# Optimization experiments

Measured on AMD Instinct MI355X. Metric: run time of the kernel, lower is better.

Reference implementation:

```python
import jax, jax.numpy as jnp
import numpy as np

N, F, H, R, B, L, C, E, NB = 8192, 512, 256, 16, 32, 256, 7, 262144, 30
D = F + H


def setup_inputs() -> dict:
    ks = jax.random.split(jax.random.key(0), 16)
    g = lambda k, shape, fan: jax.random.normal(k, shape, jnp.float32) / np.sqrt(fan)
    return {
        "x": jax.random.normal(ks[0], (N, F), jnp.float32),
        "edge_index": jax.random.randint(ks[1], (2, E), 0, N),
        "edge_norm": jax.random.uniform(ks[2], (E,), jnp.float32),
        "edge_type": jax.random.randint(ks[3], (E,), 0, R),
        "seq_lengths": jnp.full((B,), L, dtype=jnp.int32),
        "umask": jnp.ones((B, L), jnp.float32),
        "nodal_attn": 1,
        "avec": 0,
        "basis": g(ks[4], (NB, F, H), F),
        "comp": g(ks[5], (R, NB), NB),
        "root1": g(ks[6], (F, H), F),
        "bias1": jnp.zeros((H,), jnp.float32),
        "w_rel": g(ks[7], (H, H), H),
        "b_rel": jnp.zeros((H,), jnp.float32),
        "w_root": g(ks[8], (H, H), H),
        "w_att": g(ks[9], (D, D), D),
        "b_att": jnp.zeros((D,), jnp.float32),
        "w_lin": g(ks[10], (D, H), D),
        "b_lin": jnp.zeros((H,), jnp.float32),
        "w_fc": g(ks[11], (H, C), H),
        "b_fc": jnp.zeros((C,), jnp.float32),
    }


def reference(x, edge_index, edge_norm, edge_type, seq_lengths, umask,
              nodal_attn, avec, basis, comp, root1, bias1, w_rel, b_rel,
              w_root, w_att, b_att, w_lin, b_lin, w_fc, b_fc):
    n = x.shape[0]
    r = comp.shape[0]
    src, dst = edge_index[0], edge_index[1]
    # ---- RGCNConv (num_bases basis decomposition, mean aggregation per relation, root + bias)
    W = jnp.einsum('rb,bfh->rfh', comp, basis)             # [R,F,H]
    xw = jnp.einsum('nf,rfh->nrh', x, W)                   # [N,R,H]
    msg = xw[src, edge_type]                               # [E,H] gather per edge
    seg = dst * r + edge_type                              # per (node, relation) segment
    cnt = jax.ops.segment_sum(jnp.ones((msg.shape[0],), msg.dtype), seg, num_segments=n * r)
    msg = msg / jnp.maximum(cnt[seg], 1.0)[:, None]
    out1 = jax.ops.segment_sum(msg, dst, num_segments=n) + x @ root1 + bias1
    # ---- GraphConv (add aggregation): W_rel * sum_j h_j + b_rel + W_root * h_i
    agg2 = jax.ops.segment_sum(out1[src], dst, num_segments=n)
    out2 = agg2 @ w_rel + b_rel + out1 @ w_root
    emotions = jnp.concatenate([x, out2], axis=-1)          # [N, F+H]
    if int(nodal_attn):
        seq = np.asarray(seq_lengths)                       # static conversation lengths
        starts = np.concatenate([[0], np.cumsum(seq)[:-1]])
        lmax = int(seq.max())
        rows = [jnp.pad(jax.lax.dynamic_slice_in_dim(emotions, int(s), int(l)),
                        ((0, lmax - int(l)), (0, 0)))
                for s, l in zip(starts, seq)]
        M = jnp.stack(rows, 0).transpose(1, 0, 2)           # [L, B, D]
        mask = umask                                        # [B, L]
        # MatchingAttention 'general2', vectorized over all timesteps t
        X = M @ w_att + b_att                               # transform(x_t) for every t: [L,B,D]
        Mm = M * mask.T[:, :, None]                         # mask memory over seq dim
        scores = jnp.einsum('tbd,sbd->tbs', X, Mm) * mask[None]
        a = jax.nn.softmax(jnp.tanh(scores), axis=-1) * mask[None]
        a = a / jnp.sum(a, axis=-1, keepdims=True)
        att = jnp.einsum('tbs,sbd->tbd', a, M)              # [L,B,D]
        hidden = jax.nn.relu(att @ w_lin + b_lin)
    else:
        hidden = jax.nn.relu(emotions @ w_lin + b_lin)
    # dropout is identity in eval mode
    logits = hidden @ w_fc + b_fc
    if int(avec):
        return logits
    return jax.nn.log_softmax(logits, axis=1)  # faithful: torch uses dim=1
```

## Files before the change

kernel.cpp:

```cpp
#include <hip/hip_runtime.h>
#include <hip/hip_bf16.h>

#define NN 8192
#define FF 512
#define HH 256
#define RR 16
#define BB 32
#define LL 256
#define CC 7
#define EE 262144
#define NBASE 30
#define DD 768

constexpr int FLAG_BIAS = 1, FLAG_RELU = 4, FLAG_TANH = 8,
              FLAG_SPLITOUT = 16, FLAG_TAILOUT = 32, FLAG_TAIL2 = 64;

typedef __attribute__((ext_vector_type(8))) short bf16x8;
typedef __attribute__((ext_vector_type(4))) float f32x4;

__global__ __launch_bounds__(256) void detect_dtype(const unsigned short* __restrict__ xs,
                                                    int* __restrict__ flag) {
  __shared__ int red[256];
  int cnt = 0;
  for (int i = threadIdx.x * 2; i < 8192; i += 512) {
    unsigned short u = xs[i];
    int e = (u >> 7) & 0xFF;
    if (e >= 0xC0) cnt++;
  }
  red[threadIdx.x] = cnt;
  __syncthreads();
  for (int s = 128; s > 0; s >>= 1) {
    if (threadIdx.x < s) red[threadIdx.x] += red[threadIdx.x + s];
    __syncthreads();
  }
  if (threadIdx.x == 0) flag[0] = (red[0] > 16) ? 1 : 0;
}

struct PSeg {
  const void* src;
  float* dst;
  __hip_bfloat16* hi;
  __hip_bfloat16* lo;
  __hip_bfloat16* hi2;
  __hip_bfloat16* lo2;
  long n;
  int R, C, ld, off;
  int type;
  int zero;
};
struct PTable {
  PSeg seg[16];
  int count;
  long total;
};

__global__ __launch_bounds__(256) void prep_all(PTable t, const int* __restrict__ flag) {
  const int fp32 = flag[0];
  for (long i = (long)blockIdx.x * 256 + threadIdx.x; i < t.total;
       i += (long)gridDim.x * 256) {
    long off = i;
    int s = 0;
    while (off >= t.seg[s].n) { off -= t.seg[s].n; s++; }
    const PSeg& sg = t.seg[s];
    if (sg.type == 0) {
      float v = 0.f;
      if (!sg.zero)
        v = fp32 ? ((const float*)sg.src)[off]
                 : __bfloat162float(((const __hip_bfloat16*)sg.src)[off]);
      if (sg.dst) sg.dst[off] = v;
      if (sg.hi) {
        __hip_bfloat16 h = __float2bfloat16(v);
        __hip_bfloat16 l = __float2bfloat16(v - __bfloat162float(h));
        sg.hi[off] = h;
        sg.lo[off] = l;
        if (sg.hi2) {
          long d2 = (off >> 9) * DD + (off & 511);
          sg.hi2[d2] = h;
          sg.lo2[d2] = l;
        }
      }
    } else {
      int r = (int)(off % sg.R), c = (int)(off / sg.R);
      float v = fp32 ? ((const float*)sg.src)[(long)r * sg.C + c]
                     : __bfloat162float(((const __hip_bfloat16*)sg.src)[(long)r * sg.C + c]);
      __hip_bfloat16 h = __float2bfloat16(v);
      long d = (long)c * sg.ld + sg.off + r;
      sg.hi[d] = h;
      sg.lo[d] = __float2bfloat16(v - __bfloat162float(h));
    }
  }
}

__global__ __launch_bounds__(256) void wt_gemm(
    const float* __restrict__ basis, const float* __restrict__ comp,
    float* __restrict__ wt_nat) {
  __shared__ float cs[RR * NBASE];
  int tid = threadIdx.x;
  for (int i = tid; i < RR * NBASE; i += 256) cs[i] = comp[i];
  __syncthreads();
  long col = (long)blockIdx.x * 256 + tid;
  float acc[RR] = {};
  for (int b = 0; b < NBASE; ++b) {
    float v = basis[(long)b * 131072 + col];
#pragma unroll
    for (int r = 0; r < RR; ++r) acc[r] += cs[r * NBASE + b] * v;
  }
#pragma unroll
  for (int r = 0; r < RR; ++r) wt_nat[(long)r * 131072 + col] = acc[r];
}

__global__ __launch_bounds__(256) void wt_transpose(
    const float* __restrict__ wt_nat,
    __hip_bfloat16* __restrict__ hi, __hip_bfloat16* __restrict__ lo) {
  __shared__ float t[32][33];
  const int r = blockIdx.z;
  const int f0 = blockIdx.y * 32, h0 = blockIdx.x * 32;
  const int c = threadIdx.x & 31, rw = threadIdx.x >> 5;
  const float* src = wt_nat + ((long)r * 512 + f0) * 256 + h0;
#pragma unroll
  for (int i = 0; i < 4; ++i)
    t[rw + i * 8][c] = src[(long)(rw + i * 8) * 256 + c];
  __syncthreads();
#pragma unroll
  for (int i = 0; i < 4; ++i) {
    int hh = rw + i * 8;
    float v = t[c][hh];
    long orow = (long)(r * 256 + h0 + hh) * 512 + f0 + c;
    __hip_bfloat16 hv = __float2bfloat16(v);
    hi[orow] = hv;
    lo[orow] = __float2bfloat16(v - __bfloat162float(hv));
  }
}

__device__ __forceinline__ void gload_lds16(const void* g, void* l) {
  __builtin_amdgcn_global_load_lds(
      (const __attribute__((address_space(1))) unsigned int*)g,
      (__attribute__((address_space(3))) unsigned int*)l, 16, 0, 0);
}

__global__ __launch_bounds__(256, 3) void mfma_dual(
    const __hip_bfloat16* __restrict__ A, const __hip_bfloat16* __restrict__ Alo,
    const __hip_bfloat16* __restrict__ Bt, const __hip_bfloat16* __restrict__ Btlo,
    const float* __restrict__ bias, float* __restrict__ C, float* __restrict__ Ct,
    __hip_bfloat16* __restrict__ Chi, __hip_bfloat16* __restrict__ Clo,
    __hip_bfloat16* __restrict__ Chi2, __hip_bfloat16* __restrict__ Clo2,
    int K, int ldc, long sA, long sB, long sC, int flags) {
  __shared__ __hip_bfloat16 Ah[128 * 32];
  __shared__ __hip_bfloat16 Bh[128 * 32];
  __shared__ __hip_bfloat16 Al[128 * 32];
  __shared__ __hip_bfloat16 Bl[128 * 32];
  const int tid = threadIdx.x;
  const int w = tid >> 6, lane = tid & 63;
  const long z = blockIdx.z;
  const long row0 = (long)blockIdx.y * 128, col0 = (long)blockIdx.x * 128;
  const int wm = w & 1, wn = w >> 1;
  const int srow0 = (w * 128 + lane) >> 2;
  const int srow1 = (w * 128 + 64 + lane) >> 2;
  const int kch = (lane & 3) * 8;
  const int fr = lane & 15, q = lane >> 4;
  const bool hasAlo = (Alo != nullptr);
  const __hip_bfloat16* Az = A + z * sA;
  const __hip_bfloat16* Alz = hasAlo ? (Alo + z * sA) : nullptr;
  const __hip_bfloat16* Bz = Bt + z * sB;
  const __hip_bfloat16* Blz = Btlo + z * sB;
  const long aoff0 = (row0 + srow0) * K + kch, aoff1 = (row0 + srow1) * K + kch;
  const long boff0 = (col0 + srow0) * K + kch, boff1 = (col0 + srow1) * K + kch;
  f32x4 acc[4][4] = {};
  for (int k0 = 0; k0 < K; k0 += 32) {
    gload_lds16(Az + aoff0 + k0, Ah + w * 1024);
    gload_lds16(Az + aoff1 + k0, Ah + w * 1024 + 512);
    gload_lds16(Bz + boff0 + k0, Bh + w * 1024);
    gload_lds16(Bz + boff1 + k0, Bh + w * 1024 + 512);
    gload_lds16(Blz + boff0 + k0, Bl + w * 1024);
    gload_lds16(Blz + boff1 + k0, Bl + w * 1024 + 512);
    if (hasAlo) {
      gload_lds16(Alz + aoff0 + k0, Al + w * 1024);
      gload_lds16(Alz + aoff1 + k0, Al + w * 1024 + 512);
    }
    __syncthreads();
    bf16x8 ah[4], bh[4], bl[4];
#pragma unroll
    for (int i = 0; i < 4; ++i) {
      ah[i] = *(const bf16x8*)&Ah[(wm * 64 + i * 16 + fr) * 32 + q * 8];
      bh[i] = *(const bf16x8*)&Bh[(wn * 64 + i * 16 + fr) * 32 + q * 8];
      bl[i] = *(const bf16x8*)&Bl[(wn * 64 + i * 16 + fr) * 32 + q * 8];
    }
#pragma unroll
    for (int i = 0; i < 4; ++i)
#pragma unroll
      for (int j = 0; j < 4; ++j) {
        acc[i][j] = __builtin_amdgcn_mfma_f32_16x16x32_bf16(ah[i], bh[j], acc[i][j], 0, 0, 0);
        acc[i][j] = __builtin_amdgcn_mfma_f32_16x16x32_bf16(ah[i], bl[j], acc[i][j], 0, 0, 0);
      }
    if (hasAlo) {
      bf16x8 al[4];
#pragma unroll
      for (int i = 0; i < 4; ++i)
        al[i] = *(const bf16x8*)&Al[(wm * 64 + i * 16 + fr) * 32 + q * 8];
#pragma unroll
      for (int i = 0; i < 4; ++i)
#pragma unroll
        for (int j = 0; j < 4; ++j)
          acc[i][j] = __builtin_amdgcn_mfma_f32_16x16x32_bf16(al[i], bh[j], acc[i][j], 0, 0, 0);
    }
    __syncthreads();
  }
  const int cr = (lane >> 4) * 4, cc = lane & 15;
  float* Cz = C ? (C + z * sC) : nullptr;
  __hip_bfloat16* Chz = Chi ? (Chi + z * sC) : nullptr;
  __hip_bfloat16* Clz = Clo ? (Clo + z * sC) : nullptr;
#pragma unroll
  for (int i = 0; i < 4; ++i) {
    long rbase = row0 + wm * 64 + i * 16 + cr;
#pragma unroll
    for (int j = 0; j < 4; ++j) {
      long col = col0 + wn * 64 + j * 16 + cc;
      float bv = (flags & FLAG_BIAS) ? bias[col] : 0.f;
#pragma unroll
      for (int r = 0; r < 4; ++r) {
        float v = acc[i][j][r] + bv;
        if (flags & FLAG_RELU) v = fmaxf(v, 0.f);
        if (flags & FLAG_TANH) v = tanhf(v);
        long row = rbase + r;
        if ((flags & FLAG_TAIL2) && col >= 768) {
          long off2 = (row >> 8) * 65536 + (col - 768) * 256 + (row & 255);
          __hip_bfloat16 hv = __float2bfloat16(v);
          Chi2[off2] = hv;
          Clo2[off2] = __float2bfloat16(v - __bfloat162float(hv));
        } else if (flags & FLAG_SPLITOUT) {
          long off = row * ldc + col;
          __hip_bfloat16 hv = __float2bfloat16(v);
          Chz[off] = hv;
          Clz[off] = __float2bfloat16(v - __bfloat162float(hv));
        } else if ((flags & FLAG_TAILOUT) && col >= 4096) {
          Ct[row * 256 + (col - 4096)] = v;
        } else {
          Cz[row * ldc + col] = v;
        }
      }
    }
  }
}

__global__ __launch_bounds__(256) void count_edges(
    const int* __restrict__ ei, const int* __restrict__ et, float* __restrict__ cnt) {
  int e = blockIdx.x * 256 + threadIdx.x;
  if (e < EE) atomicAdd(&cnt[ei[EE + e] * RR + et[e]], 1.0f);
}

__global__ __launch_bounds__(256) void scan_rowptr(
    const float* __restrict__ cntf, int* __restrict__ rowptr, int* __restrict__ fill) {
  __shared__ int part[256];
  int tid = threadIdx.x;
  int base = tid * 32;
  int local[32];
  int s = 0;
  for (int i = 0; i < 32; ++i) {
    local[i] = s;
    const float* c = &cntf[(base + i) * RR];
    int d = 0;
#pragma unroll
    for (int r = 0; r < RR; ++r) d += (int)c[r];
    s += d;
  }
  part[tid] = s;
  __syncthreads();
  for (int off = 1; off < 256; off <<= 1) {
    int v = (tid >= off) ? part[tid - off] : 0;
    __syncthreads();
    part[tid] += v;
    __syncthreads();
  }
  int prev = (tid == 0) ? 0 : part[tid - 1];
  for (int i = 0; i < 32; ++i) rowptr[base + i] = prev + local[i];
  if (tid == 255) rowptr[8192] = part[255];
  for (int i = tid; i < 8192; i += 256) fill[i] = 0;
}

__global__ __launch_bounds__(256) void edge_fill(
    const int* __restrict__ ei, const int* __restrict__ et,
    const int* __restrict__ rowptr, int* __restrict__ fill, int* __restrict__ eidx) {
  int e = blockIdx.x * 256 + threadIdx.x;
  if (e < EE) {
    int dst = ei[EE + e];
    int pos = rowptr[dst] + atomicAdd(&fill[dst], 1);
    eidx[pos] = ei[e] | (et[e] << 16);
  }
}

__global__ __launch_bounds__(256) void rgcn_gather(
    const int* __restrict__ rowptr, const int* __restrict__ eidx,
    const float* __restrict__ cntf, const float* __restrict__ xw,
    float* __restrict__ out1, __hip_bfloat16* __restrict__ a2o1_hi,
    __hip_bfloat16* __restrict__ a2o1_lo) {
  const int dst = blockIdx.x;
  const int h = threadIdx.x;
  __shared__ float inv[RR];
  __shared__ int se[256];
  if (h < RR) inv[h] = 1.0f / fmaxf(cntf[dst * RR + h], 1.0f);
  const int beg = rowptr[dst], end = rowptr[dst + 1];
  float a0 = 0.f, a1 = 0.f, a2 = 0.f, a3 = 0.f;
  for (int c0 = beg; c0 < end; c0 += 256) {
    int n = min(256, end - c0);
    __syncthreads();
    if (h < n) se[h] = eidx[c0 + h];
    __syncthreads();
    int i = 0;
    for (; i + 4 <= n; i += 4) {
      int p0 = se[i], p1 = se[i + 1], p2 = se[i + 2], p3 = se[i + 3];
      float v0 = xw[((long)(p0 & 0xFFFF) << 12) + ((p0 >> 16) << 8) + h];
      float v1 = xw[((long)(p1 & 0xFFFF) << 12) + ((p1 >> 16) << 8) + h];
      float v2 = xw[((long)(p2 & 0xFFFF) << 12) + ((p2 >> 16) << 8) + h];
      float v3 = xw[((long)(p3 & 0xFFFF) << 12) + ((p3 >> 16) << 8) + h];
      a0 += v0 * inv[p0 >> 16];
      a1 += v1 * inv[p1 >> 16];
      a2 += v2 * inv[p2 >> 16];
      a3 += v3 * inv[p3 >> 16];
    }
    for (; i < n; ++i) {
      int pk = se[i];
      a0 += xw[((long)(pk & 0xFFFF) << 12) + ((pk >> 16) << 8) + h] * inv[pk >> 16];
    }
  }
  float tot = out1[((long)dst << 8) + h] + ((a0 + a1) + (a2 + a3));
  out1[((long)dst << 8) + h] = tot;
  __hip_bfloat16 hv = __float2bfloat16(tot);
  long d = (long)dst * 512 + 256 + h;
  a2o1_hi[d] = hv;
  a2o1_lo[d] = __float2bfloat16(tot - __bfloat162float(hv));
}

__global__ __launch_bounds__(256) void graphconv_gather(
    const int* __restrict__ rowptr, const int* __restrict__ eidx,
    const float* __restrict__ out1, __hip_bfloat16* __restrict__ a2o1_hi,
    __hip_bfloat16* __restrict__ a2o1_lo) {
  const int dst = blockIdx.x;
  const int h = threadIdx.x;
  __shared__ int se[256];
  const int beg = rowptr[dst], end = rowptr[dst + 1];
  float a0 = 0.f, a1 = 0.f, a2 = 0.f, a3 = 0.f;
  for (int c0 = beg; c0 < end; c0 += 256) {
    int n = min(256, end - c0);
    __syncthreads();
    if (h < n) se[h] = eidx[c0 + h];
    __syncthreads();
    int i = 0;
    for (; i + 4 <= n; i += 4) {
      a0 += out1[((long)(se[i] & 0xFFFF) << 8) + h];
      a1 += out1[((long)(se[i + 1] & 0xFFFF) << 8) + h];
      a2 += out1[((long)(se[i + 2] & 0xFFFF) << 8) + h];
      a3 += out1[((long)(se[i + 3] & 0xFFFF) << 8) + h];
    }
    for (; i < n; ++i) a0 += out1[((long)(se[i] & 0xFFFF) << 8) + h];
  }
  float acc = (a0 + a1) + (a2 + a3);
  __hip_bfloat16 hv = __float2bfloat16(acc);
  long d = (long)dst * 512 + h;
  a2o1_hi[d] = hv;
  a2o1_lo[d] = __float2bfloat16(acc - __bfloat162float(hv));
}

__global__ __launch_bounds__(256) void softmax256(const float* __restrict__ S,
                                                  __hip_bfloat16* __restrict__ Ab) {
  __shared__ float red[256];
  long row = blockIdx.x;
  const float* p = S + row * 256;
  int t = threadIdx.x;
  float v = p[t];
  red[t] = v;
  __syncthreads();
  for (int s = 128; s > 0; s >>= 1) {
    if (t < s) red[t] = fmaxf(red[t], red[t + s]);
    __syncthreads();
  }
  float m = red[0];
  __syncthreads();
  float e = __expf(v - m);
  red[t] = e;
  __syncthreads();
  for (int s = 128; s > 0; s >>= 1) {
    if (t < s) red[t] += red[t + s];
    __syncthreads();
  }
  Ab[row * 256 + t] = __float2bfloat16(e / red[0]);
}

__global__ __launch_bounds__(256) void logits_lsm(
    const float* __restrict__ hidden, const float* __restrict__ w_fc,
    const float* __restrict__ b_fc, void* __restrict__ out_v,
    const int* __restrict__ flag) {
  __shared__ float wf[256 * 7];
  __shared__ float lg[224];
  __shared__ float corr[7];
  int t = blockIdx.x;
  int tid = threadIdx.x;
  for (int i = tid; i < 256 * 7; i += 256) wf[i] = w_fc[i];
  __syncthreads();
  if (tid < 224) {
    int b = tid / 7, c = tid % 7;
    const float* hr = hidden + ((long)((b << 8) + t) << 8);
    float s = b_fc[c];
    for (int k = 0; k < 256; ++k) s += hr[k] * wf[k * 7 + c];
    lg[tid] = s;
  }
  __syncthreads();
  if (tid < 7) {
    float m = -1e30f;
    for (int b = 0; b < BB; ++b) m = fmaxf(m, lg[b * 7 + tid]);
    float sum = 0.f;
    for (int b = 0; b < BB; ++b) sum += __expf(lg[b * 7 + tid] - m);
    corr[tid] = m + logf(sum);
  }
  __syncthreads();
  if (tid < 224) {
    float v = lg[tid] - corr[tid % 7];
    if (flag[0]) ((float*)out_v)[t * 224 + tid] = v;
    else ((__hip_bfloat16*)out_v)[t * 224 + tid] = __float2bfloat16(v);
  }
}

extern "C" void kernel_launch(void* const* d_in, const int* in_sizes, int n_in,
                              void* d_out, int out_size, void* d_ws, size_t ws_size,
                              hipStream_t stream) {
  const int* ei = (const int*)d_in[1];
  const int* et = (const int*)d_in[3];

  float* ws = (float*)d_ws;
  int* flag = (int*)d_ws;
  float* p = ws + 16;
  auto alloc = [&](long nf) { float* r = p; p += nf; return r; };
  float* w_fc_f = alloc(1792);
  float* b_rel_f = alloc(256);
  float* biasx = alloc(4352);
  float* battx = alloc(1024);
  float* b_lin_f = alloc(256);
  float* b_fc_f = alloc(16);
  __hip_bfloat16* x_hi = (__hip_bfloat16*)alloc(2097152);
  __hip_bfloat16* x_lo = (__hip_bfloat16*)alloc(2097152);
  __hip_bfloat16* wae_hi = (__hip_bfloat16*)alloc(393216);
  __hip_bfloat16* wae_lo = (__hip_bfloat16*)alloc(393216);
  __hip_bfloat16* wrr_hi = (__hip_bfloat16*)alloc(65536);
  __hip_bfloat16* wrr_lo = (__hip_bfloat16*)alloc(65536);
  __hip_bfloat16* wtc_hi = (__hip_bfloat16*)alloc(1114112);
  __hip_bfloat16* wtc_lo = (__hip_bfloat16*)alloc(1114112);
  float* basis_f = alloc(3932160);
  float* comp_f = alloc(512);
  float* xw = alloc(33554432);
  float* cnt = alloc(131072);
  float* out1 = alloc(2097152);
  __hip_bfloat16* a2o1_hi = (__hip_bfloat16*)alloc(2097152);
  __hip_bfloat16* a2o1_lo = (__hip_bfloat16*)alloc(2097152);
  float* hidden = alloc(2097152);
  int* rowptr = (int*)alloc(8208);
  int* fillc = (int*)alloc(8192);
  int* eidx = (int*)alloc(262144);
  float* wt_nat = xw;
  float* em = xw;
  __hip_bfloat16* emwT_hi = (__hip_bfloat16*)(em + 2097152);
  __hip_bfloat16* emwT_lo = (__hip_bfloat16*)(em + 3145728);
  __hip_bfloat16* em_hi = (__hip_bfloat16*)(em + 6291456);
  __hip_bfloat16* em_lo = (__hip_bfloat16*)(em + 9437184);
  __hip_bfloat16* X_hi = (__hip_bfloat16*)(em + 12582912);
  __hip_bfloat16* X_lo = (__hip_bfloat16*)(em + 15728640);
  float* scores = em + 18874368;
  __hip_bfloat16* a_b16 = (__hip_bfloat16*)(em + 20971520);

  detect_dtype<<<1, 256, 0, stream>>>((const unsigned short*)d_in[0], flag);
  PTable T{};
  long tot = 0;
  int ns = 0;
  auto segL = [&](const void* s, float* d, __hip_bfloat16* hi, __hip_bfloat16* lo,
                  __hip_bfloat16* hi2, __hip_bfloat16* lo2, long n, int z) {
    T.seg[ns] = PSeg{s, d, hi, lo, hi2, lo2, n, 0, 0, 0, 0, 0, z};
    ns++; tot += n;
  };
  auto segT = [&](const void* s, __hip_bfloat16* hi, __hip_bfloat16* lo,
                  int R, int C, int ld, int off) {
    T.seg[ns] = PSeg{s, nullptr, hi, lo, nullptr, nullptr, (long)R * C, R, C, ld, off, 1, 0};
    ns++; tot += (long)R * C;
  };
  segL(d_in[0], nullptr, x_hi, x_lo, nullptr, nullptr, NN * FF, 0);
  segL(d_in[8], basis_f, nullptr, nullptr, nullptr, nullptr, NBASE * FF * HH, 0);
  segL(d_in[9], comp_f, nullptr, nullptr, nullptr, nullptr, RR * NBASE, 0);
  segL(d_in[13], b_rel_f, nullptr, nullptr, nullptr, nullptr, HH, 0);
  segL(d_in[16], battx, nullptr, nullptr, nullptr, nullptr, DD, 0);
  segL(nullptr, battx + DD, nullptr, nullptr, nullptr, nullptr, 256, 1);
  segL(d_in[18], b_lin_f, nullptr, nullptr, nullptr, nullptr, HH, 0);
  segL(d_in[19], w_fc_f, nullptr, nullptr, nullptr, nullptr, HH * CC, 0);
  segL(d_in[20], b_fc_f, nullptr, nullptr, nullptr, nullptr, CC, 0);
  segL(nullptr, biasx, nullptr, nullptr, nullptr, nullptr, 4096, 1);
  segL(d_in[11], biasx + 4096, nullptr, nullptr, nullptr, nullptr, HH, 0);
  segT(d_in[15], wae_hi, wae_lo, DD, DD, DD, 0);
  segT(d_in[17], wae_hi + 768 * 768, wae_lo + 768 * 768, DD, HH, DD, 0);
  segT(d_in[10], wtc_hi + 4096 * 512, wtc_lo + 4096 * 512, FF, HH, FF, 0);
  segT(d_in[12], wrr_hi, wrr_lo, HH, HH, 512, 0);
  segT(d_in[14], wrr_hi, wrr_lo, HH, HH, 512, 256);
  T.count = ns;
  T.total = tot;
  prep_all<<<4096, 256, 0, stream>>>(T, flag);

  wt_gemm<<<131072 / 256, 256, 0, stream>>>(basis_f, comp_f, wt_nat);
  wt_transpose<<<dim3(8, 16, 16), 256, 0, stream>>>(wt_nat, wtc_hi, wtc_lo);
  mfma_dual<<<dim3(34, 64, 1), 256, 0, stream>>>(
      x_hi, x_lo, wtc_hi, wtc_lo, biasx, xw, out1, nullptr, nullptr, nullptr, nullptr,
      FF, 4096, 0, 0, 0, FLAG_BIAS | FLAG_TAILOUT);
  hipMemsetAsync(cnt, 0, 131072 * sizeof(float), stream);
  count_edges<<<EE / 256, 256, 0, stream>>>(ei, et, cnt);
  scan_rowptr<<<1, 256, 0, stream>>>(cnt, rowptr, fillc);
  edge_fill<<<EE / 256, 256, 0, stream>>>(ei, et, rowptr, fillc, eidx);
  rgcn_gather<<<NN, 256, 0, stream>>>(rowptr, eidx, cnt, xw, out1, a2o1_hi, a2o1_lo);
  graphconv_gather<<<NN, 256, 0, stream>>>(rowptr, eidx, out1, a2o1_hi, a2o1_lo);
  {
    PTable T2{};
    T2.seg[0] = PSeg{nullptr, nullptr, nullptr, nullptr, nullptr, nullptr,
                     (long)NN * FF, 0, 0, 0, 0, 2, 0};
  }
  {
    struct { const __hip_bfloat16 *xh, *xl; __hip_bfloat16 *eh, *el; } args{x_hi, x_lo, em_hi, em_lo};
  }
  extern __global__ void copy_xsplit_k(const __hip_bfloat16*, const __hip_bfloat16*,
                                       __hip_bfloat16*, __hip_bfloat16*);
  copy_xsplit_k<<<(NN * FF) / 256, 256, 0, stream>>>(x_hi, x_lo, em_hi, em_lo);
  mfma_dual<<<dim3(2, 64, 1), 256, 0, stream>>>(
      a2o1_hi, a2o1_lo, wrr_hi, wrr_lo, b_rel_f, nullptr, nullptr,
      em_hi + 512, em_lo + 512, nullptr, nullptr, 512, DD, 0, 0, 0,
      FLAG_BIAS | FLAG_SPLITOUT);
  mfma_dual<<<dim3(8, 64, 1), 256, 0, stream>>>(
      em_hi, em_lo, wae_hi, wae_lo, battx, nullptr, nullptr, X_hi, X_lo,
      emwT_hi, emwT_lo, DD, DD, 0, 0, 0, FLAG_BIAS | FLAG_SPLITOUT | FLAG_TAIL2);
  mfma_dual<<<dim3(2, 2, BB), 256, 0, stream>>>(
      X_hi, X_lo, em_hi, em_lo, nullptr, scores, nullptr, nullptr, nullptr,
      nullptr, nullptr, DD, LL, (long)LL * DD, (long)LL * DD, (long)LL * LL, FLAG_TANH);
  softmax256<<<BB * LL, 256, 0, stream>>>(scores, a_b16);
  mfma_dual<<<dim3(2, 2, BB), 256, 0, stream>>>(
      a_b16, nullptr, emwT_hi, emwT_lo, b_lin_f, hidden, nullptr, nullptr, nullptr,
      nullptr, nullptr, LL, HH, (long)LL * LL, (long)LL * HH, (long)LL * HH,
      FLAG_BIAS | FLAG_RELU);
  logits_lsm<<<LL, 256, 0, stream>>>(hidden, w_fc_f, b_fc_f, d_out, flag);
}

__global__ __launch_bounds__(256) void copy_xsplit_k(
    const __hip_bfloat16* __restrict__ xh, const __hip_bfloat16* __restrict__ xl,
    __hip_bfloat16* __restrict__ eh, __hip_bfloat16* __restrict__ el) {
  int idx = blockIdx.x * 256 + threadIdx.x;
  int n = idx >> 9, f = idx & 511;
  long d = (long)n * DD + f;
  eh[d] = xh[idx];
  el[d] = xl[idx];
}
```

Baseline: 616.3 us.

## Add 256x256-tile 8-wave split-bf16 MFMA GEMM with pipelined LDS loads for big GEMMs

Introduces mfma_dual8, a 512-thread kernel computing 256x256 output tiles with three bf16 MFMA passes (hi*hi, hi*lo, lo*hi), double-buffered direct global-to-LDS loads interleaved with compute phases, XOR-swizzled LDS reads, setprio around MFMA bursts and a grid swizzle for L2 locality. It replaces the older kernel for the two largest GEMMs (x times the relation weights and the attention transform), aiming to raise data reuse per tile and overlap memory with math. It also removes some dead scaffolding blocks. The larger tile gives fewer workgroups (544 and 128), which may leave some CUs idle and adds register pressure.

```diff
diff --git a/kernel.cpp b/kernel.cpp
--- a/kernel.cpp
+++ b/kernel.cpp
@@ -236,6 +236,143 @@
           Ct[row * 256 + (col - 4096)] = v;
         } else {
           Cz[row * ldc + col] = v;
+        }
+      }
+    }
+  }
+}
+
+__device__ __forceinline__ void rd4(bf16x8 (&d)[4], const __hip_bfloat16* t,
+                                    int rbase, int ro) {
+#pragma unroll
+  for (int i = 0; i < 4; ++i)
+    d[i] = *(const bf16x8*)&t[(rbase + i * 16) * 32 + ro];
+}
+
+__device__ __forceinline__ void mm16(f32x4 (&acc)[8][4], int g,
+                                     const bf16x8 (&a)[4], const bf16x8 (&b)[4]) {
+#pragma unroll
+  for (int i = 0; i < 4; ++i)
+#pragma unroll
+    for (int j = 0; j < 4; ++j)
+      acc[g * 4 + i][j] =
+          __builtin_amdgcn_mfma_f32_16x16x32_bf16(a[i], b[j], acc[g * 4 + i][j], 0, 0, 0);
+}
+
+#define P_TAIL(g_)                                   \
+  __builtin_amdgcn_s_barrier();                      \
+  asm volatile("s_waitcnt lgkmcnt(0)" ::: "memory"); \
+  __builtin_amdgcn_sched_barrier(0);                 \
+  __builtin_amdgcn_s_setprio(1);                     \
+  mm16(acc, g_, af, bf);                             \
+  __builtin_amdgcn_s_setprio(0);
+
+__global__ __launch_bounds__(512, 2) void mfma_dual8(
+    const __hip_bfloat16* __restrict__ A, const __hip_bfloat16* __restrict__ Alo,
+    const __hip_bfloat16* __restrict__ Bt, const __hip_bfloat16* __restrict__ Btlo,
+    const float* __restrict__ bias, float* __restrict__ C, float* __restrict__ Ct,
+    __hip_bfloat16* __restrict__ Chi, __hip_bfloat16* __restrict__ Clo,
+    __hip_bfloat16* __restrict__ Chi2, __hip_bfloat16* __restrict__ Clo2,
+    int K, int ldc, int NT, int flags) {
+  __shared__ __hip_bfloat16 sm[2][4][256 * 32];
+  const int tid = threadIdx.x;
+  const int w = tid >> 6, lane = tid & 63;
+  const int wm = w >> 2, wn = w & 3;
+  const int nwg = gridDim.x * gridDim.y;
+  const int bid = blockIdx.y * gridDim.x + blockIdx.x;
+  const int swz = (bid & 7) * (nwg >> 3) + (bid >> 3);
+  const int ty = swz % gridDim.y, tx = swz / gridDim.y;
+  const long row0 = (long)ty * 256, col0 = (long)tx * 256;
+  const int urow = tid >> 2;
+  const int qg = (tid & 3) ^ ((tid >> 3) & 3);
+  const long ga0 = (row0 + urow) * (long)K + qg * 8, ga1 = ga0 + 128L * K;
+  const long gb0 = (col0 + urow) * (long)K + qg * 8, gb1 = gb0 + 128L * K;
+  const int fr = lane & 15, q = lane >> 4;
+  const int ro = fr * 32 + ((q ^ ((fr >> 1) & 3)) << 3);
+  const int arow = wm * 128, brow = wn * 64;
+  const int lw = w * 512;
+  f32x4 acc[8][4] = {};
+
+  gload_lds16(A + ga0, &sm[0][0][lw]);
+  gload_lds16(A + ga1, &sm[0][0][4096 + lw]);
+  gload_lds16(Bt + gb0, &sm[0][1][lw]);
+  gload_lds16(Bt + gb1, &sm[0][1][4096 + lw]);
+  gload_lds16(Alo + ga0, &sm[0][2][lw]);
+  gload_lds16(Alo + ga1, &sm[0][2][4096 + lw]);
+  gload_lds16(Btlo + gb0, &sm[0][3][lw]);
+  gload_lds16(Btlo + gb1, &sm[0][3][4096 + lw]);
+  asm volatile("s_waitcnt vmcnt(4)" ::: "memory");
+  __builtin_amdgcn_s_barrier();
+
+  for (int t = 0; t < NT; ++t) {
+    const int cur = t & 1, nxt = cur ^ 1;
+    const long kn = (long)((t + 1 < NT) ? t + 1 : t) << 5;
+    const __hip_bfloat16* sA = sm[cur][0];
+    const __hip_bfloat16* sB = sm[cur][1];
+    const __hip_bfloat16* sAl = sm[cur][2];
+    const __hip_bfloat16* sBl = sm[cur][3];
+    bf16x8 af[4], bf[4];
+    rd4(af, sA, arow, ro);
+    rd4(bf, sB, brow, ro);
+    gload_lds16(A + ga0 + kn, &sm[nxt][0][lw]);
+    gload_lds16(A + ga1 + kn, &sm[nxt][0][4096 + lw]);
+    P_TAIL(0);
+    __builtin_amdgcn_s_barrier();
+    rd4(af, sA, arow + 64, ro);
+    gload_lds16(Bt + gb0 + kn, &sm[nxt][1][lw]);
+    gload_lds16(Bt + gb1 + kn, &sm[nxt][1][4096 + lw]);
+    P_TAIL(1);
+    asm volatile("s_waitcnt vmcnt(4)" ::: "memory");
+    __builtin_amdgcn_s_barrier();
+    rd4(af, sA, arow, ro);
+    rd4(bf, sBl, brow, ro);
+    gload_lds16(Alo + ga0 + kn, &sm[nxt][2][lw]);
+    gload_lds16(Alo + ga1 + kn, &sm[nxt][2][4096 + lw]);
+    P_TAIL(0);
+    __builtin_amdgcn_s_barrier();
+    rd4(af, sA, arow + 64, ro);
+    gload_lds16(Btlo + gb0 + kn, &sm[nxt][3][lw]);
+    gload_lds16(Btlo + gb1 + kn, &sm[nxt][3][4096 + lw]);
+    P_TAIL(1);
+    __builtin_amdgcn_s_barrier();
+    rd4(af, sAl, arow, ro);
+    rd4(bf, sB, brow, ro);
+    P_TAIL(0);
+    __builtin_amdgcn_s_barrier();
+    rd4(af, sAl, arow + 64, ro);
+    P_TAIL(1);
+    asm volatile("s_waitcnt vmcnt(4)" ::: "memory");
+    __builtin_amdgcn_s_barrier();
+  }
+  asm volatile("s_waitcnt vmcnt(0)" ::: "memory");
+
+  const int cr = q * 4, cc = fr;
+#pragma unroll
+  for (int i = 0; i < 8; ++i) {
+    long rbase = row0 + wm * 128 + i * 16 + cr;
+#pragma unroll
+    for (int j = 0; j < 4; ++j) {
+      long col = col0 + wn * 64 + j * 16 + cc;
+      float bv = (flags & FLAG_BIAS) ? bias[col] : 0.f;
+#pragma unroll
+      for (int r = 0; r < 4; ++r) {
+        float v = acc[i][j][r] + bv;
+        if (flags & FLAG_RELU) v = fmaxf(v, 0.f);
+        long row = rbase + r;
+        if ((flags & FLAG_TAIL2) && col >= 768) {
+          long off2 = (row >> 8) * 65536 + (col - 768) * 256 + (row & 255);
+          __hip_bfloat16 hv = __float2bfloat16(v);
+          Chi2[off2] = hv;
+          Clo2[off2] = __float2bfloat16(v - __bfloat162float(hv));
+        } else if (flags & FLAG_SPLITOUT) {
+          long off = row * ldc + col;
+          __hip_bfloat16 hv = __float2bfloat16(v);
+          Chi[off] = hv;
+          Clo[off] = __float2bfloat16(v - __bfloat162float(hv));
+        } else if ((flags & FLAG_TAILOUT) && col >= 4096) {
+          Ct[row * 256 + (col - 4096)] = v;
+        } else {
+          C[row * ldc + col] = v;
         }
       }
     }
@@ -501,23 +638,15 @@
 
   wt_gemm<<<131072 / 256, 256, 0, stream>>>(basis_f, comp_f, wt_nat);
   wt_transpose<<<dim3(8, 16, 16), 256, 0, stream>>>(wt_nat, wtc_hi, wtc_lo);
-  mfma_dual<<<dim3(34, 64, 1), 256, 0, stream>>>(
+  mfma_dual8<<<dim3(17, 32), 512, 0, stream>>>(
       x_hi, x_lo, wtc_hi, wtc_lo, biasx, xw, out1, nullptr, nullptr, nullptr, nullptr,
-      FF, 4096, 0, 0, 0, FLAG_BIAS | FLAG_TAILOUT);
+      FF, 4096, FF / 32, FLAG_BIAS | FLAG_TAILOUT);
   hipMemsetAsync(cnt, 0, 131072 * sizeof(float), stream);
   count_edges<<<EE / 256, 256, 0, stream>>>(ei, et, cnt);
   scan_rowptr<<<1, 256, 0, stream>>>(cnt, rowptr, fillc);
   edge_fill<<<EE / 256, 256, 0, stream>>>(ei, et, rowptr, fillc, eidx);
   rgcn_gather<<<NN, 256, 0, stream>>>(rowptr, eidx, cnt, xw, out1, a2o1_hi, a2o1_lo);
   graphconv_gather<<<NN, 256, 0, stream>>>(rowptr, eidx, out1, a2o1_hi, a2o1_lo);
-  {
-    PTable T2{};
-    T2.seg[0] = PSeg{nullptr, nullptr, nullptr, nullptr, nullptr, nullptr,
-                     (long)NN * FF, 0, 0, 0, 0, 2, 0};
-  }
-  {
-    struct { const __hip_bfloat16 *xh, *xl; __hip_bfloat16 *eh, *el; } args{x_hi, x_lo, em_hi, em_lo};
-  }
   extern __global__ void copy_xsplit_k(const __hip_bfloat16*, const __hip_bfloat16*,
                                        __hip_bfloat16*, __hip_bfloat16*);
   copy_xsplit_k<<<(NN * FF) / 256, 256, 0, stream>>>(x_hi, x_lo, em_hi, em_lo);
@@ -525,9 +654,9 @@
       a2o1_hi, a2o1_lo, wrr_hi, wrr_lo, b_rel_f, nullptr, nullptr,
       em_hi + 512, em_lo + 512, nullptr, nullptr, 512, DD, 0, 0, 0,
       FLAG_BIAS | FLAG_SPLITOUT);
-  mfma_dual<<<dim3(8, 64, 1), 256, 0, stream>>>(
+  mfma_dual8<<<dim3(4, 32), 512, 0, stream>>>(
       em_hi, em_lo, wae_hi, wae_lo, battx, nullptr, nullptr, X_hi, X_lo,
-      emwT_hi, emwT_lo, DD, DD, 0, 0, 0, FLAG_BIAS | FLAG_SPLITOUT | FLAG_TAIL2);
+      emwT_hi, emwT_lo, DD, DD, DD / 32, FLAG_BIAS | FLAG_SPLITOUT | FLAG_TAIL2);
   mfma_dual<<<dim3(2, 2, BB), 256, 0, stream>>>(
       X_hi, X_lo, em_hi, em_lo, nullptr, scores, nullptr, nullptr, nullptr,
       nullptr, nullptr, DD, LL, (long)LL * DD, (long)LL * DD, (long)LL * LL, FLAG_TANH);
```

After: 719.9 us. 16.8% more time.
